# Kernel tuning notes

Hardware: AMD Instinct MI355X
Metric: run time of the kernel (lower is better)

Reference implementation:

```python
import jax, jax.numpy as jnp
import numpy as np

H, KD, VD = 12, 64, 64  # num_heads, k_dim, v_dim
EPS = 1e-12

def _l2norm(x, axis):
    n = jnp.linalg.norm(x, axis=axis, keepdims=True)
    return x / jnp.maximum(n, EPS)

def setup_inputs() -> dict:
    key = jax.random.key(0)
    ks = jax.random.split(key, 6)
    d1, d2 = 768, 768
    return {
        "x1": jax.random.normal(ks[0], (2048, d1), jnp.float32),
        "x2": jax.random.normal(ks[1], (8192, d2), jnp.float32),
        "Wq": jax.random.normal(ks[2], (H * KD, d1), jnp.float32) * 0.03,
        "Wk": jax.random.normal(ks[3], (H * KD, d2), jnp.float32) * 0.03,
        "Wv": jax.random.normal(ks[4], (H * VD, d2), jnp.float32) * 0.03,
        "Wo": jax.random.normal(ks[5], (d1, H * VD), jnp.float32) * 0.03,
        "invt": 20,
    }

def reference(x1, x2, Wq, Wk, Wv, Wo, invt):
    B1 = x1.shape[0]
    B2 = x2.shape[0]
    # Linear (no bias): y = x @ W.T, then split heads
    q = (x1 @ Wq.T).reshape(B1, H, KD)  # [B1,H,KD]
    k = (x2 @ Wk.T).reshape(B2, H, KD)  # [B2,H,KD]
    v = (x2 @ Wv.T).reshape(B2, H, VD)  # [B2,H,VD]
    # per-head L2 normalization over feature dim (cosine attention)
    q = _l2norm(q, axis=-1)
    k = _l2norm(k, axis=-1)
    attn = jnp.einsum("bhd,nhd->hbn", q, k) * jnp.float32(invt)  # [H,B1,B2]
    attn = jax.nn.softmax(attn, axis=-1)
    out = jnp.einsum("hbn,nhd->bhd", attn, v).reshape(B1, H * VD)
    out = out @ Wo.T  # [B1, in_dim1]
    return _l2norm(out, axis=1)
```

## Files before the change

### kernel.cpp

```cpp
#include <hip/hip_runtime.h>
#include <hip/hip_bf16.h>
#include <math.h>

#define B1 2048
#define B2 8192
#define NH 12
#define DH 64
#define DMODEL 768

typedef __attribute__((ext_vector_type(8))) short short8;
typedef __attribute__((ext_vector_type(4))) float floatx4;
typedef __attribute__((ext_vector_type(8))) unsigned short ushort8;
typedef __attribute__((ext_vector_type(4))) unsigned short ushort4v;

static __device__ __forceinline__ unsigned short f2bf(float f) {
  __bf16 b = (__bf16)f;
  return __builtin_bit_cast(unsigned short, b);
}
static __device__ __forceinline__ float bf2f(unsigned short u) {
  return __builtin_bit_cast(float, ((unsigned)u) << 16);
}

static __device__ __forceinline__ void gload16(const unsigned short* g,
                                               unsigned short* l) {
  __builtin_amdgcn_global_load_lds(
      (const __attribute__((address_space(1))) void*)g,
      (__attribute__((address_space(3))) void*)l, 16, 0, 0);
}

__global__ __launch_bounds__(256) void prep_all(
    const float* __restrict__ x1, unsigned short* __restrict__ x1h,
    unsigned short* __restrict__ x1l, const float* __restrict__ x2,
    unsigned short* __restrict__ x2h, unsigned short* __restrict__ x2l,
    const float* __restrict__ Wq, unsigned short* __restrict__ Wqh,
    unsigned short* __restrict__ Wql, const float* __restrict__ Wk,
    unsigned short* __restrict__ Wkh, unsigned short* __restrict__ Wkl,
    const float* __restrict__ Wv, unsigned short* __restrict__ Wvh,
    const float* __restrict__ Wo, unsigned short* __restrict__ Woh) {
  const int bi = blockIdx.x;
  const float* src;
  unsigned short *hi, *lo = nullptr;
  int lb;
  if (bi < 1536) {
    src = x1; hi = x1h; lo = x1l; lb = bi;
  } else if (bi < 7680) {
    src = x2; hi = x2h; lo = x2l; lb = bi - 1536;
  } else if (bi < 8256) {
    src = Wq; hi = Wqh; lo = Wql; lb = bi - 7680;
  } else if (bi < 8832) {
    src = Wk; hi = Wkh; lo = Wkl; lb = bi - 8256;
  } else if (bi < 9408) {
    src = Wv; hi = Wvh; lb = bi - 8832;
  } else {
    src = Wo; hi = Woh; lb = bi - 9408;
  }
  const int i = (lb * 256 + threadIdx.x) * 4;
  const float4 v = *(const float4*)&src[i];
  ushort4v h = {f2bf(v.x), f2bf(v.y), f2bf(v.z), f2bf(v.w)};
  *(ushort4v*)&hi[i] = h;
  if (lo) {
    ushort4v l = {f2bf(v.x - bf2f(h[0])), f2bf(v.y - bf2f(h[1])),
                  f2bf(v.z - bf2f(h[2])), f2bf(v.w - bf2f(h[3]))};
    *(ushort4v*)&lo[i] = l;
  }
}

template <bool SPLIT, bool L2N, bool F32OUT>
static __device__ __forceinline__ void gemm_tile(
    const unsigned short* __restrict__ Ahg, const unsigned short* __restrict__ Alg,
    const unsigned short* __restrict__ Bhg, const unsigned short* __restrict__ Blg,
    void* __restrict__ Cv, int M, int N, int K, int m0, int n0,
    unsigned short* sAh, unsigned short* sBh, unsigned short* sAl,
    unsigned short* sBl) {
  const int tid = threadIdx.x;
  const int wave = tid >> 6;
  const int lane = tid & 63;
  const int wm = wave >> 1;
  const int wn = wave & 1;
  const int n15 = lane & 15;
  const int quad = lane >> 4;
  const int srow = lane >> 2;
  const int cpl = (lane & 3) ^ (srow >> 2);

  floatx4 acc[4][4];
#pragma unroll
  for (int i = 0; i < 4; ++i)
#pragma unroll
    for (int j = 0; j < 4; ++j) acc[i][j] = (floatx4){0.f, 0.f, 0.f, 0.f};

  for (int k0 = 0; k0 < K; k0 += 32) {
    __syncthreads();
#pragma unroll
    for (int jj = 0; jj < 2; ++jj) {
      const int j = wave * 2 + jj;
      const int row = j * 16 + srow;
      const size_t goffA = (size_t)(m0 + row) * K + k0 + cpl * 8;
      const size_t goffB = (size_t)(n0 + row) * K + k0 + cpl * 8;
      gload16(Ahg + goffA, &sAh[j * 512]);
      gload16(Bhg + goffB, &sBh[j * 512]);
      if constexpr (SPLIT) {
        gload16(Alg + goffA, &sAl[j * 512]);
        gload16(Blg + goffB, &sBl[j * 512]);
      }
    }
    __syncthreads();

    short8 afh[4], afl[4];
#pragma unroll
    for (int mt = 0; mt < 4; ++mt) {
      const int row = wm * 64 + mt * 16 + n15;
      const int off = row * 32 + ((quad ^ (n15 >> 2)) << 3);
      afh[mt] = *(const short8*)&sAh[off];
      if constexpr (SPLIT) afl[mt] = *(const short8*)&sAl[off];
    }
#pragma unroll
    for (int nt = 0; nt < 4; ++nt) {
      const int row = wn * 64 + nt * 16 + n15;
      const int off = row * 32 + ((quad ^ (n15 >> 2)) << 3);
      const short8 bfh = *(const short8*)&sBh[off];
      if constexpr (SPLIT) {
        const short8 bfl = *(const short8*)&sBl[off];
#pragma unroll
        for (int mt = 0; mt < 4; ++mt) {
          acc[mt][nt] = __builtin_amdgcn_mfma_f32_16x16x32_bf16(afh[mt], bfh, acc[mt][nt], 0, 0, 0);
          acc[mt][nt] = __builtin_amdgcn_mfma_f32_16x16x32_bf16(afh[mt], bfl, acc[mt][nt], 0, 0, 0);
          acc[mt][nt] = __builtin_amdgcn_mfma_f32_16x16x32_bf16(afl[mt], bfh, acc[mt][nt], 0, 0, 0);
        }
      } else {
#pragma unroll
        for (int mt = 0; mt < 4; ++mt)
          acc[mt][nt] = __builtin_amdgcn_mfma_f32_16x16x32_bf16(afh[mt], bfh, acc[mt][nt], 0, 0, 0);
      }
    }
  }

#pragma unroll
  for (int mt = 0; mt < 4; ++mt) {
    float scalev[4] = {1.f, 1.f, 1.f, 1.f};
    if constexpr (L2N) {
#pragma unroll
      for (int rr = 0; rr < 4; ++rr) {
        float ss = 0.f;
#pragma unroll
        for (int nt = 0; nt < 4; ++nt) ss += acc[mt][nt][rr] * acc[mt][nt][rr];
        ss += __shfl_xor(ss, 1, 64);
        ss += __shfl_xor(ss, 2, 64);
        ss += __shfl_xor(ss, 4, 64);
        ss += __shfl_xor(ss, 8, 64);
        scalev[rr] = 1.0f / fmaxf(sqrtf(ss), 1e-12f);
      }
    }
#pragma unroll
    for (int nt = 0; nt < 4; ++nt) {
#pragma unroll
      for (int rr = 0; rr < 4; ++rr) {
        const int row = m0 + wm * 64 + mt * 16 + quad * 4 + rr;
        const int col = n0 + wn * 64 + nt * 16 + n15;
        const float v = acc[mt][nt][rr] * scalev[rr];
        if constexpr (F32OUT)
          ((float*)Cv)[(size_t)row * N + col] = v;
        else
          ((unsigned short*)Cv)[(size_t)row * N + col] = f2bf(v);
      }
    }
  }
}

__global__ __launch_bounds__(256) void qk_proj(
    const unsigned short* __restrict__ x1h, const unsigned short* __restrict__ x1l,
    const unsigned short* __restrict__ Wqh, const unsigned short* __restrict__ Wql,
    const unsigned short* __restrict__ x2h, const unsigned short* __restrict__ x2l,
    const unsigned short* __restrict__ Wkh, const unsigned short* __restrict__ Wkl,
    unsigned short* __restrict__ qbf, unsigned short* __restrict__ kbf) {
  __shared__ __align__(16) unsigned short sAh[4096], sBh[4096], sAl[4096], sBl[4096];
  const int bi = blockIdx.x;
  if (bi < 96) {
    gemm_tile<true, true, false>(x1h, x1l, Wqh, Wql, qbf, B1, DMODEL, DMODEL,
                                 (bi / 6) * 128, (bi % 6) * 128, sAh, sBh, sAl, sBl);
  } else {
    const int b = bi - 96;
    gemm_tile<true, true, false>(x2h, x2l, Wkh, Wkl, kbf, B2, DMODEL, DMODEL,
                                 (b / 6) * 128, (b % 6) * 128, sAh, sBh, sAl, sBl);
  }
}

__global__ __launch_bounds__(256) void v_proj(
    const unsigned short* __restrict__ Wvh, const unsigned short* __restrict__ x2h,
    unsigned short* __restrict__ vtbf) {
  __shared__ __align__(16) unsigned short sAh[4096], sBh[4096];
  const int bi = blockIdx.x;
  gemm_tile<false, false, false>(Wvh, nullptr, x2h, nullptr, vtbf, DMODEL, B2,
                                 DMODEL, (bi / 64) * 128, (bi % 64) * 128,
                                 sAh, sBh, nullptr, nullptr);
}

#define KC 128
#define KSPLIT 2
#define NCH (B2 / KSPLIT / KC)
#define PSTR 68

__global__ __launch_bounds__(256, 3) void attn_mfma(
    const unsigned short* __restrict__ qb, const unsigned short* __restrict__ kb,
    const unsigned short* __restrict__ vt, float* __restrict__ aoacc,
    float* __restrict__ lacc, const int* __restrict__ invt_p) {
  __shared__ __align__(16) unsigned short smem[25088];
  unsigned short* Psl = smem + 16384;

  const int bid = blockIdx.x;
  const int swz = (bid & 7) * 96 + (bid >> 3);
  const int zz = swz / 384;
  const int rem = swz - zz * 384;
  const int h = rem >> 5;
  const int q0 = (rem & 31) * 64;

  const float c2 = (float)invt_p[0] * 1.4426950408889634f;
  const int tid = threadIdx.x;
  const int wave = tid >> 6;
  const int lane = tid & 63;
  const int qsub = wave >> 1;
  const int ksub = wave & 1;
  const int n15 = lane & 15;
  const int quad = lane >> 4;
  const int kz0 = zz * (B2 / KSPLIT);

  unsigned short* Ps = &Psl[wave * 32 * PSTR];

  short8 qf[2][2];
#pragma unroll
  for (int qt = 0; qt < 2; ++qt)
#pragma unroll
    for (int ks = 0; ks < 2; ++ks) {
      const int qrow = q0 + qsub * 32 + qt * 16 + n15;
      qf[qt][ks] = *(const short8*)&qb[(size_t)qrow * DMODEL + h * DH + ks * 32 + quad * 8];
    }

  floatx4 oacc[2][4];
#pragma unroll
  for (int qt = 0; qt < 2; ++qt)
#pragma unroll
    for (int nt = 0; nt < 4; ++nt) oacc[qt][nt] = (floatx4){0.f, 0.f, 0.f, 0.f};
  float lsum[2] = {0.f, 0.f};

  const unsigned short* kbp = kb + (size_t)kz0 * DMODEL + h * DH;
  const unsigned short* vbp = vt + (size_t)(h * DH) * B2 + kz0;

  ushort8 kr[4];
#pragma unroll
  for (int i = 0; i < 4; ++i) {
    const int s = i * 256 + tid;
    const int key = s >> 3, cpk = s & 7, chk = cpk ^ (key & 7);
    kr[i] = *(const ushort8*)&kbp[(size_t)key * DMODEL + chk * 8];
  }
#pragma unroll
  for (int i = 0; i < 4; ++i) {
    const int s = i * 256 + tid;
    const int key = s >> 3, cpk = s & 7;
    *(ushort8*)&smem[key * 64 + cpk * 8] = kr[i];
  }
#pragma unroll
  for (int i = 0; i < 4; ++i) {
    const int s = i * 256 + tid;
    const int key = s >> 3, cpk = s & 7, chk = cpk ^ (key & 7);
    kr[i] = *(const ushort8*)&kbp[(size_t)(KC + key) * DMODEL + chk * 8];
  }
  __syncthreads();

  for (int c = 0; c < NCH; ++c) {
    unsigned short* Kb = &smem[(c & 1) * 8192];
    unsigned short* Kn = &smem[((c + 1) & 1) * 8192];
    const unsigned short* vc_ = vbp + c * KC;

    ushort8 vr[8];
#pragma unroll
    for (int ks = 0; ks < 2; ++ks)
#pragma unroll
      for (int nt = 0; nt < 4; ++nt)
        vr[ks * 4 + nt] = *(const ushort8*)&vc_[
            (size_t)(nt * 16 + n15) * B2 + (ksub * 8 + ks * 4 + quad) * 8];

    if (c + 1 < NCH) {
#pragma unroll
      for (int i = 0; i < 4; ++i) {
        const int s = i * 256 + tid;
        const int key = s >> 3, cpk = s & 7;
        *(ushort8*)&Kn[key * 64 + cpk * 8] = kr[i];
      }
      if (c + 2 < NCH) {
        const unsigned short* k2 = kbp + (size_t)(c + 2) * KC * DMODEL;
#pragma unroll
        for (int i = 0; i < 4; ++i) {
          const int s = i * 256 + tid;
          const int key = s >> 3, cpk = s & 7, chk = cpk ^ (key & 7);
          kr[i] = *(const ushort8*)&k2[(size_t)key * DMODEL + chk * 8];
        }
      }
    }

#pragma unroll
    for (int kt = 0; kt < 4; ++kt) {
      floatx4 s0 = {0.f, 0.f, 0.f, 0.f}, s1 = {0.f, 0.f, 0.f, 0.f};
#pragma unroll
      for (int ks = 0; ks < 2; ++ks) {
        const int key = ksub * 64 + kt * 16 + n15;
        const int cp = (ks * 4 + quad) ^ (n15 & 7);
        const short8 kf = *(const short8*)&Kb[key * 64 + cp * 8];
        s0 = __builtin_amdgcn_mfma_f32_16x16x32_bf16(kf, qf[0][ks], s0, 0, 0, 0);
        s1 = __builtin_amdgcn_mfma_f32_16x16x32_bf16(kf, qf[1][ks], s1, 0, 0, 0);
      }
      ushort4v p0, p1;
#pragma unroll
      for (int r = 0; r < 4; ++r) {
        const float e0 = exp2f(fmaf(s0[r], c2, -c2));
        const float e1 = exp2f(fmaf(s1[r], c2, -c2));
        lsum[0] += e0;
        lsum[1] += e1;
        p0[r] = f2bf(e0);
        p1[r] = f2bf(e1);
      }
      *(ushort4v*)&Ps[(0 * 16 + n15) * PSTR + kt * 16 + quad * 4] = p0;
      *(ushort4v*)&Ps[(1 * 16 + n15) * PSTR + kt * 16 + quad * 4] = p1;
    }

#pragma unroll
    for (int ks = 0; ks < 2; ++ks) {
      short8 pa[2];
#pragma unroll
      for (int qt = 0; qt < 2; ++qt)
        pa[qt] = *(const short8*)&Ps[(qt * 16 + n15) * PSTR + ks * 32 + quad * 8];
#pragma unroll
      for (int nt = 0; nt < 4; ++nt) {
        const short8 vf = __builtin_bit_cast(short8, vr[ks * 4 + nt]);
        oacc[0][nt] = __builtin_amdgcn_mfma_f32_16x16x32_bf16(pa[0], vf, oacc[0][nt], 0, 0, 0);
        oacc[1][nt] = __builtin_amdgcn_mfma_f32_16x16x32_bf16(pa[1], vf, oacc[1][nt], 0, 0, 0);
      }
    }

    __syncthreads();
  }

#pragma unroll
  for (int qt = 0; qt < 2; ++qt) {
    float v = lsum[qt];
    v += __shfl_xor(v, 16, 64);
    v += __shfl_xor(v, 32, 64);
    lsum[qt] = v;
  }

  float* aoz = aoacc + (size_t)zz * B1 * DMODEL;
  float* lz = lacc + (size_t)zz * B1 * NH;

  __syncthreads();
  float* Osc = (float*)smem;
  float* lsc = Osc + 4096;
  if (ksub == 1) {
#pragma unroll
    for (int qt = 0; qt < 2; ++qt)
#pragma unroll
      for (int nt = 0; nt < 4; ++nt)
#pragma unroll
        for (int r = 0; r < 4; ++r) {
          const int row = qsub * 32 + qt * 16 + quad * 4 + r;
          Osc[row * 64 + nt * 16 + n15] = oacc[qt][nt][r];
        }
    if (quad == 0) {
      lsc[qsub * 32 + n15] = lsum[0];
      lsc[qsub * 32 + 16 + n15] = lsum[1];
    }
  }
  __syncthreads();
  if (ksub == 0) {
#pragma unroll
    for (int qt = 0; qt < 2; ++qt)
#pragma unroll
      for (int nt = 0; nt < 4; ++nt)
#pragma unroll
        for (int r = 0; r < 4; ++r) {
          const int row = qsub * 32 + qt * 16 + quad * 4 + r;
          const float v = oacc[qt][nt][r] + Osc[row * 64 + nt * 16 + n15];
          aoz[(size_t)(q0 + row) * DMODEL + h * DH + nt * 16 + n15] = v;
        }
    if (quad == 0) {
      lz[(size_t)(q0 + qsub * 32 + n15) * NH + h] = lsum[0] + lsc[qsub * 32 + n15];
      lz[(size_t)(q0 + qsub * 32 + 16 + n15) * NH + h] =
          lsum[1] + lsc[qsub * 32 + 16 + n15];
    }
  }
}

__global__ __launch_bounds__(256) void wo_proj(
    const float* __restrict__ aoacc, const float* __restrict__ lacc,
    const unsigned short* __restrict__ Woh, float* __restrict__ woout) {
  __shared__ __align__(16) unsigned short sAh[4096], sBh[4096];
  const int bi = blockIdx.x;
  const int m0 = (bi / 6) * 128;
  const int n0 = (bi % 6) * 128;
  const int tid = threadIdx.x;
  const int wave = tid >> 6;
  const int lane = tid & 63;
  const int wm = wave >> 1;
  const int wn = wave & 1;
  const int n15 = lane & 15;
  const int quad = lane >> 4;
  const int srow = lane >> 2;
  const int cpl = (lane & 3) ^ (srow >> 2);

  const float* ao1 = aoacc + (size_t)B1 * DMODEL;
  const float* la1 = lacc + (size_t)B1 * NH;

  floatx4 acc[4][4];
#pragma unroll
  for (int i = 0; i < 4; ++i)
#pragma unroll
    for (int j = 0; j < 4; ++j) acc[i][j] = (floatx4){0.f, 0.f, 0.f, 0.f};

  for (int k0 = 0; k0 < DMODEL; k0 += 32) {
    __syncthreads();
#pragma unroll
    for (int jj = 0; jj < 2; ++jj) {
      const int j = wave * 2 + jj;
      const int row = j * 16 + srow;
      const size_t ga = (size_t)(m0 + row) * DMODEL + k0 + cpl * 8;
      const float4 a0 = *(const float4*)&aoacc[ga];
      const float4 a1 = *(const float4*)&aoacc[ga + 4];
      const float4 b0 = *(const float4*)&ao1[ga];
      const float4 b1 = *(const float4*)&ao1[ga + 4];
      const int head = (k0 + cpl * 8) >> 6;
      const float lsum = lacc[(m0 + row) * NH + head] + la1[(m0 + row) * NH + head];
      const float inv = 1.0f / lsum;
      ushort8 ah = {f2bf((a0.x + b0.x) * inv), f2bf((a0.y + b0.y) * inv),
                    f2bf((a0.z + b0.z) * inv), f2bf((a0.w + b0.w) * inv),
                    f2bf((a1.x + b1.x) * inv), f2bf((a1.y + b1.y) * inv),
                    f2bf((a1.z + b1.z) * inv), f2bf((a1.w + b1.w) * inv)};
      *(ushort8*)&sAh[j * 512 + lane * 8] = ah;
      gload16(Woh + (size_t)(n0 + row) * DMODEL + k0 + cpl * 8, &sBh[j * 512]);
    }
    __syncthreads();

    short8 afh[4];
#pragma unroll
    for (int mt = 0; mt < 4; ++mt) {
      const int row = wm * 64 + mt * 16 + n15;
      afh[mt] = *(const short8*)&sAh[row * 32 + ((quad ^ (n15 >> 2)) << 3)];
    }
#pragma unroll
    for (int nt = 0; nt < 4; ++nt) {
      const int row = wn * 64 + nt * 16 + n15;
      const short8 bfh = *(const short8*)&sBh[row * 32 + ((quad ^ (n15 >> 2)) << 3)];
#pragma unroll
      for (int mt = 0; mt < 4; ++mt)
        acc[mt][nt] = __builtin_amdgcn_mfma_f32_16x16x32_bf16(afh[mt], bfh, acc[mt][nt], 0, 0, 0);
    }
  }

#pragma unroll
  for (int mt = 0; mt < 4; ++mt)
#pragma unroll
    for (int nt = 0; nt < 4; ++nt)
#pragma unroll
      for (int rr = 0; rr < 4; ++rr) {
        const int row = m0 + wm * 64 + mt * 16 + quad * 4 + rr;
        const int col = n0 + wn * 64 + nt * 16 + n15;
        woout[(size_t)row * DMODEL + col] = acc[mt][nt][rr];
      }
}

__global__ __launch_bounds__(256) void l2norm_rows768_out(
    const float* __restrict__ x, float* __restrict__ out) {
  const int row = blockIdx.x;
  const float* xr = &x[(size_t)row * DMODEL];
  float ss = 0.0f;
  float vals[3];
#pragma unroll
  for (int i = 0; i < 3; ++i) {
    vals[i] = xr[threadIdx.x + i * 256];
    ss += vals[i] * vals[i];
  }
#pragma unroll
  for (int off = 32; off > 0; off >>= 1) ss += __shfl_xor(ss, off, 64);
  __shared__ float ws[4];
  if ((threadIdx.x & 63) == 0) ws[threadIdx.x >> 6] = ss;
  __syncthreads();
  const float tot = ws[0] + ws[1] + ws[2] + ws[3];
  const float sc = 1.0f / fmaxf(sqrtf(tot), 1e-12f);
  float* orow = &out[(size_t)row * DMODEL];
#pragma unroll
  for (int i = 0; i < 3; ++i) orow[threadIdx.x + i * 256] = vals[i] * sc;
}

extern "C" void kernel_launch(void* const* d_in, const int* in_sizes, int n_in,
                              void* d_out, int out_size, void* d_ws,
                              size_t ws_size, hipStream_t stream) {
  const float* x1 = (const float*)d_in[0];
  const float* x2 = (const float*)d_in[1];
  const float* Wq = (const float*)d_in[2];
  const float* Wk = (const float*)d_in[3];
  const float* Wv = (const float*)d_in[4];
  const float* Wo = (const float*)d_in[5];
  const int* invt = (const int*)d_in[6];
  float* outp = (float*)d_out;

  char* ws = (char*)d_ws;
  unsigned short* x1h = (unsigned short*)(ws + 0);
  unsigned short* x1l = (unsigned short*)(ws + 3145728);
  unsigned short* x2h = (unsigned short*)(ws + 6291456);
  unsigned short* x2l = (unsigned short*)(ws + 18874368);
  unsigned short* Wqh = (unsigned short*)(ws + 31457280);
  unsigned short* Wql = (unsigned short*)(ws + 32636928);
  unsigned short* Wkh = (unsigned short*)(ws + 33816576);
  unsigned short* Wkl = (unsigned short*)(ws + 34996224);
  unsigned short* Wvh = (unsigned short*)(ws + 36175872);
  unsigned short* Woh = (unsigned short*)(ws + 37355520);
  unsigned short* q_bf = (unsigned short*)(ws + 38535168);
  unsigned short* k_bf = (unsigned short*)(ws + 41680896);
  float* aoacc = (float*)(ws + 0);
  float* lacc = (float*)(ws + 32636928);
  unsigned short* vt_bf = (unsigned short*)(ws + 18874368);
  float* woout = (float*)(ws + 12582912);

  prep_all<<<9984, 256, 0, stream>>>(x1, x1h, x1l, x2, x2h, x2l, Wq, Wqh, Wql,
                                     Wk, Wkh, Wkl, Wv, Wvh, Wo, Woh);
  qk_proj<<<480, 256, 0, stream>>>(x1h, x1l, Wqh, Wql, x2h, x2l, Wkh, Wkl,
                                   q_bf, k_bf);
  v_proj<<<384, 256, 0, stream>>>(Wvh, x2h, vt_bf);
  attn_mfma<<<768, 256, 0, stream>>>(q_bf, k_bf, vt_bf, aoacc, lacc, invt);
  wo_proj<<<96, 256, 0, stream>>>(aoacc, lacc, Woh, woout);
  l2norm_rows768_out<<<B1, 256, 0, stream>>>(woout, outp);
}
```

Measured before the change: 318.2 us.

## Drop activation low-part split and fuse Q/K/V projections into one kernel

Stops producing and consuming the bf16 low-order residual of x1 and x2, so the split-precision GEMM uses two MFMA products (Ah*Bh + Ah*Bl) instead of three. This removes the residual writes in prep, their loads and LDS traffic, and a third of the projection MFMAs. The V projection is merged into the Q/K projection launch, removing a kernel boundary. The exchange is lower accuracy of the q/k projections, since activation rounding error is no longer compensated.

```diff
diff --git a/kernel.cpp b/kernel.cpp
--- a/kernel.cpp
+++ b/kernel.cpp
@@ -30,8 +30,7 @@
 
 __global__ __launch_bounds__(256) void prep_all(
     const float* __restrict__ x1, unsigned short* __restrict__ x1h,
-    unsigned short* __restrict__ x1l, const float* __restrict__ x2,
-    unsigned short* __restrict__ x2h, unsigned short* __restrict__ x2l,
+    const float* __restrict__ x2, unsigned short* __restrict__ x2h,
     const float* __restrict__ Wq, unsigned short* __restrict__ Wqh,
     unsigned short* __restrict__ Wql, const float* __restrict__ Wk,
     unsigned short* __restrict__ Wkh, unsigned short* __restrict__ Wkl,
@@ -42,9 +41,9 @@
   unsigned short *hi, *lo = nullptr;
   int lb;
   if (bi < 1536) {
-    src = x1; hi = x1h; lo = x1l; lb = bi;
+    src = x1; hi = x1h; lb = bi;
   } else if (bi < 7680) {
-    src = x2; hi = x2h; lo = x2l; lb = bi - 1536;
+    src = x2; hi = x2h; lb = bi - 1536;
   } else if (bi < 8256) {
     src = Wq; hi = Wqh; lo = Wql; lb = bi - 7680;
   } else if (bi < 8832) {
@@ -65,13 +64,13 @@
   }
 }
 
-template <bool SPLIT, bool L2N, bool F32OUT>
+template <bool BSPLIT, bool L2N, bool F32OUT>
 static __device__ __forceinline__ void gemm_tile(
-    const unsigned short* __restrict__ Ahg, const unsigned short* __restrict__ Alg,
-    const unsigned short* __restrict__ Bhg, const unsigned short* __restrict__ Blg,
+    const unsigned short* __restrict__ Ahg,
+    const unsigned short* __restrict__ Bhg,
+    const unsigned short* __restrict__ Blg,
     void* __restrict__ Cv, int M, int N, int K, int m0, int n0,
-    unsigned short* sAh, unsigned short* sBh, unsigned short* sAl,
-    unsigned short* sBl) {
+    unsigned short* sAh, unsigned short* sBh, unsigned short* sBl) {
   const int tid = threadIdx.x;
   const int wave = tid >> 6;
   const int lane = tid & 63;
@@ -98,33 +97,30 @@
       const size_t goffB = (size_t)(n0 + row) * K + k0 + cpl * 8;
       gload16(Ahg + goffA, &sAh[j * 512]);
       gload16(Bhg + goffB, &sBh[j * 512]);
-      if constexpr (SPLIT) {
-        gload16(Alg + goffA, &sAl[j * 512]);
+      if constexpr (BSPLIT) {
         gload16(Blg + goffB, &sBl[j * 512]);
       }
     }
     __syncthreads();
 
-    short8 afh[4], afl[4];
+    short8 afh[4];
 #pragma unroll
     for (int mt = 0; mt < 4; ++mt) {
       const int row = wm * 64 + mt * 16 + n15;
       const int off = row * 32 + ((quad ^ (n15 >> 2)) << 3);
       afh[mt] = *(const short8*)&sAh[off];
-      if constexpr (SPLIT) afl[mt] = *(const short8*)&sAl[off];
     }
 #pragma unroll
     for (int nt = 0; nt < 4; ++nt) {
       const int row = wn * 64 + nt * 16 + n15;
       const int off = row * 32 + ((quad ^ (n15 >> 2)) << 3);
       const short8 bfh = *(const short8*)&sBh[off];
-      if constexpr (SPLIT) {
+      if constexpr (BSPLIT) {
         const short8 bfl = *(const short8*)&sBl[off];
 #pragma unroll
         for (int mt = 0; mt < 4; ++mt) {
           acc[mt][nt] = __builtin_amdgcn_mfma_f32_16x16x32_bf16(afh[mt], bfh, acc[mt][nt], 0, 0, 0);
           acc[mt][nt] = __builtin_amdgcn_mfma_f32_16x16x32_bf16(afh[mt], bfl, acc[mt][nt], 0, 0, 0);
-          acc[mt][nt] = __builtin_amdgcn_mfma_f32_16x16x32_bf16(afl[mt], bfh, acc[mt][nt], 0, 0, 0);
         }
       } else {
 #pragma unroll
@@ -166,32 +162,28 @@
   }
 }
 
-__global__ __launch_bounds__(256) void qk_proj(
-    const unsigned short* __restrict__ x1h, const unsigned short* __restrict__ x1l,
+__global__ __launch_bounds__(256) void qkv_proj(
+    const unsigned short* __restrict__ x1h,
     const unsigned short* __restrict__ Wqh, const unsigned short* __restrict__ Wql,
-    const unsigned short* __restrict__ x2h, const unsigned short* __restrict__ x2l,
+    const unsigned short* __restrict__ x2h,
     const unsigned short* __restrict__ Wkh, const unsigned short* __restrict__ Wkl,
-    unsigned short* __restrict__ qbf, unsigned short* __restrict__ kbf) {
-  __shared__ __align__(16) unsigned short sAh[4096], sBh[4096], sAl[4096], sBl[4096];
+    const unsigned short* __restrict__ Wvh,
+    unsigned short* __restrict__ qbf, unsigned short* __restrict__ kbf,
+    unsigned short* __restrict__ vtbf) {
+  __shared__ __align__(16) unsigned short sAh[4096], sBh[4096], sBl[4096];
   const int bi = blockIdx.x;
   if (bi < 96) {
-    gemm_tile<true, true, false>(x1h, x1l, Wqh, Wql, qbf, B1, DMODEL, DMODEL,
-                                 (bi / 6) * 128, (bi % 6) * 128, sAh, sBh, sAl, sBl);
+    gemm_tile<true, true, false>(x1h, Wqh, Wql, qbf, B1, DMODEL, DMODEL,
+                                 (bi / 6) * 128, (bi % 6) * 128, sAh, sBh, sBl);
+  } else if (bi < 480) {
+    const int b = bi - 96;
+    gemm_tile<true, true, false>(x2h, Wkh, Wkl, kbf, B2, DMODEL, DMODEL,
+                                 (b / 6) * 128, (b % 6) * 128, sAh, sBh, sBl);
   } else {
-    const int b = bi - 96;
-    gemm_tile<true, true, false>(x2h, x2l, Wkh, Wkl, kbf, B2, DMODEL, DMODEL,
-                                 (b / 6) * 128, (b % 6) * 128, sAh, sBh, sAl, sBl);
-  }
-}
-
-__global__ __launch_bounds__(256) void v_proj(
-    const unsigned short* __restrict__ Wvh, const unsigned short* __restrict__ x2h,
-    unsigned short* __restrict__ vtbf) {
-  __shared__ __align__(16) unsigned short sAh[4096], sBh[4096];
-  const int bi = blockIdx.x;
-  gemm_tile<false, false, false>(Wvh, nullptr, x2h, nullptr, vtbf, DMODEL, B2,
-                                 DMODEL, (bi / 64) * 128, (bi % 64) * 128,
-                                 sAh, sBh, nullptr, nullptr);
+    const int b = bi - 480;
+    gemm_tile<false, false, false>(Wvh, x2h, nullptr, vtbf, DMODEL, B2, DMODEL,
+                                   (b / 64) * 128, (b % 64) * 128, sAh, sBh, sBl);
+  }
 }
 
 #define KC 128
@@ -501,9 +493,7 @@
 
   char* ws = (char*)d_ws;
   unsigned short* x1h = (unsigned short*)(ws + 0);
-  unsigned short* x1l = (unsigned short*)(ws + 3145728);
   unsigned short* x2h = (unsigned short*)(ws + 6291456);
-  unsigned short* x2l = (unsigned short*)(ws + 18874368);
   unsigned short* Wqh = (unsigned short*)(ws + 31457280);
   unsigned short* Wql = (unsigned short*)(ws + 32636928);
   unsigned short* Wkh = (unsigned short*)(ws + 33816576);
@@ -517,11 +507,10 @@
   unsigned short* vt_bf = (unsigned short*)(ws + 18874368);
   float* woout = (float*)(ws + 12582912);
 
-  prep_all<<<9984, 256, 0, stream>>>(x1, x1h, x1l, x2, x2h, x2l, Wq, Wqh, Wql,
+  prep_all<<<9984, 256, 0, stream>>>(x1, x1h, x2, x2h, Wq, Wqh, Wql,
                                      Wk, Wkh, Wkl, Wv, Wvh, Wo, Woh);
-  qk_proj<<<480, 256, 0, stream>>>(x1h, x1l, Wqh, Wql, x2h, x2l, Wkh, Wkl,
-                                   q_bf, k_bf);
-  v_proj<<<384, 256, 0, stream>>>(Wvh, x2h, vt_bf);
+  qkv_proj<<<864, 256, 0, stream>>>(x1h, Wqh, Wql, x2h, Wkh, Wkl, Wvh,
+                                    q_bf, k_bf, vt_bf);
   attn_mfma<<<768, 256, 0, stream>>>(q_bf, k_bf, vt_bf, aoacc, lacc, invt);
   wo_proj<<<96, 256, 0, stream>>>(aoacc, lacc, Woh, woout);
   l2norm_rows768_out<<<B1, 256, 0, stream>>>(woout, outp);
```

Measured after the change: 294.6 us. 7.4% less time.
